# Performance work log

Hardware: AMD Instinct MI355X
Metric: run time of the kernel (lower is better)

Reference implementation:

```python
import jax, jax.numpy as jnp
import numpy as np

B, C, H, W = 64, 3, 64, 64
F = 96          # base_filters
K = 8           # n_mixtures
h, w = H // 2, W // 2
C0 = 2 * C      # channels of each checkerboard half
SECTIONS = [C0, C0, C0 * K, C0 * K, C0 * K]
SPLITS = [int(s) for s in np.cumsum(SECTIONS)[:-1]]
EPS = 1e-6


def conv2d(x, wgt, b):
    y = jax.lax.conv_general_dilated(x, wgt, (1, 1), 'SAME',
                                     dimension_numbers=('NCHW', 'OIHW', 'NCHW'))
    return y + b[None, :, None, None]


def layer_norm(x, g, b, eps=1e-5):
    # nn.LayerNorm(mid_shape): normalize over (C,H,W) per sample
    mu = jnp.mean(x, axis=(1, 2, 3), keepdims=True)
    var = jnp.var(x, axis=(1, 2, 3), keepdims=True)
    return (x - mu) / jnp.sqrt(var + eps) * g[None] + b[None]


def checker_split(z, odd=False):
    Bz, Cz, Hz, Wz = z.shape
    z = z.reshape(Bz, Cz, Hz // 2, 2, Wz // 2, 2)
    p00 = z[:, :, :, 0, :, 0]; p01 = z[:, :, :, 0, :, 1]
    p10 = z[:, :, :, 1, :, 0]; p11 = z[:, :, :, 1, :, 1]
    z0 = jnp.concatenate([p00, p11], axis=1)  # even checkerboard
    z1 = jnp.concatenate([p01, p10], axis=1)  # odd checkerboard
    if odd:
        z0, z1 = z1, z0
    return z0, z1


def checker_merge(z0, z1, odd=False):
    if odd:
        z0, z1 = z1, z0
    Cz = z0.shape[1] // 2
    p00, p11 = z0[:, :Cz], z0[:, Cz:]
    p01, p10 = z1[:, :Cz], z1[:, Cz:]
    Bz, _, hz, wz = p00.shape
    zi = jnp.stack([jnp.stack([p00, p01], axis=-1),
                    jnp.stack([p10, p11], axis=-1)], axis=-2)  # (B,C,h,w,2i,2j)
    z = zi.transpose(0, 1, 2, 4, 3, 5).reshape(Bz, Cz, 2 * hz, 2 * wz)
    return z


def gated_attn(x, qkv_w, qkv_b, proj_w, proj_b):
    Bx, Fx, hx, wx = x.shape
    xf = x.reshape(Bx, Fx, hx * wx).transpose(0, 2, 1)  # (B, L, F)
    qkv = xf @ qkv_w.T + qkv_b
    q, k, v = jnp.split(qkv, 3, axis=-1)
    scores = jnp.einsum('bqf,bkf->bqk', q, k) / jnp.sqrt(jnp.float32(Fx))
    attn = jax.nn.softmax(scores, axis=-1)
    o = jnp.einsum('bqk,bkf->bqf', attn, v)
    g = o @ proj_w.T + proj_b
    ga, gb = jnp.split(g, 2, axis=-1)
    out = xf + ga * jax.nn.sigmoid(gb)  # gated residual
    return out.transpose(0, 2, 1).reshape(Bx, Fx, hx, wx)


def conditioner(z1, conv1_w, conv1_b, gconv_w, gconv_b, ln1_g, ln1_b,
                qkv_w, qkv_b, proj_w, proj_b, ln2_g, ln2_b, conv2_w, conv2_b):
    x = conv2d(z1, conv1_w, conv1_b)
    g = conv2d(x, gconv_w, gconv_b)
    ga, gb = jnp.split(g, 2, axis=1)
    x = x + ga * jax.nn.sigmoid(gb)          # GatedConv2d
    x = layer_norm(x, ln1_g, ln1_b)
    x = gated_attn(x, qkv_w, qkv_b, proj_w, proj_b)
    x = layer_norm(x, ln2_g, ln2_b)
    return conv2d(x, conv2_w, conv2_b)


def _forward(z, log_df_dz, conv1_w, conv1_b, gconv_w, gconv_b, ln1_g, ln1_b,
             qkv_w, qkv_b, proj_w, proj_b, ln2_g, ln2_b, conv2_w, conv2_b,
             a_log_scale, a_bias):
    z0, z1 = checker_split(z)
    params = conditioner(z1, conv1_w, conv1_b, gconv_w, gconv_b, ln1_g, ln1_b,
                         qkv_w, qkv_b, proj_w, proj_b, ln2_g, ln2_b, conv2_w, conv2_b)
    a, b, logpi, mu, s = jnp.split(params, SPLITS, axis=1)
    a = jnp.tanh(a) * a_log_scale + a_bias
    Bz = z0.shape[0]
    logpi = jax.nn.log_softmax(logpi.reshape(Bz, K, C0, h, w), axis=1)
    mu = mu.reshape(Bz, K, C0, h, w)
    s = s.reshape(Bz, K, C0, h, w)
    # mixture-of-logistics CDF
    u = (z0[:, None] - mu) * jnp.exp(-s)
    x = jnp.sum(jnp.exp(logpi) * jax.nn.sigmoid(u), axis=1)
    log_pdf = jax.scipy.special.logsumexp(
        logpi - s + jax.nn.log_sigmoid(u) + jax.nn.log_sigmoid(-u), axis=1)
    log_df_dz = log_df_dz + jnp.sum(log_pdf.reshape(Bz, -1), axis=1)
    # logit transform
    x = jnp.clip(x, EPS, 1.0 - EPS)
    z0n = jnp.log(x) - jnp.log1p(-x)
    log_df_dz = log_df_dz + jnp.sum((-jnp.log(x) - jnp.log1p(-x)).reshape(Bz, -1), axis=1)
    # affine rescale
    z0n = z0n * jnp.exp(a) + b
    log_df_dz = log_df_dz + jnp.sum(a.reshape(Bz, -1), axis=1)
    return checker_merge(z0n, z1), log_df_dz


def setup_inputs() -> dict:
    key = jax.random.key(0)
    ks = jax.random.split(key, 10)
    sc = 0.05
    return dict(
        z=jax.random.normal(ks[0], (B, C, H, W), jnp.float32),
        log_df_dz=jnp.zeros((B,), jnp.float32),
        conv1_w=sc * jax.random.normal(ks[1], (F, C0, 3, 3), jnp.float32),
        conv1_b=jnp.zeros((F,), jnp.float32),
        gconv_w=sc * jax.random.normal(ks[2], (2 * F, F, 3, 3), jnp.float32),
        gconv_b=jnp.zeros((2 * F,), jnp.float32),
        ln1_g=jnp.ones((F, h, w), jnp.float32),
        ln1_b=jnp.zeros((F, h, w), jnp.float32),
        qkv_w=sc * jax.random.normal(ks[3], (3 * F, F), jnp.float32),
        qkv_b=jnp.zeros((3 * F,), jnp.float32),
        proj_w=sc * jax.random.normal(ks[4], (2 * F, F), jnp.float32),
        proj_b=jnp.zeros((2 * F,), jnp.float32),
        ln2_g=jnp.ones((F, h, w), jnp.float32),
        ln2_b=jnp.zeros((F, h, w), jnp.float32),
        conv2_w=sc * jax.random.normal(ks[5], (sum(SECTIONS), F, 3, 3), jnp.float32),
        conv2_b=jnp.zeros((sum(SECTIONS),), jnp.float32),
        a_log_scale=0.01 * jax.random.normal(ks[6], (1,), jnp.float32),
        a_bias=0.01 * jax.random.normal(ks[7], (1,), jnp.float32),
    )


def reference(z, log_df_dz, conv1_w, conv1_b, gconv_w, gconv_b, ln1_g, ln1_b,
              qkv_w, qkv_b, proj_w, proj_b, ln2_g, ln2_b, conv2_w, conv2_b,
              a_log_scale, a_bias):
    return _forward(z, log_df_dz, conv1_w, conv1_b, gconv_w, gconv_b, ln1_g, ln1_b,
                    qkv_w, qkv_b, proj_w, proj_b, ln2_g, ln2_b, conv2_w, conv2_b,
                    a_log_scale, a_bias)
```

## Files before the change

### kernel.cpp

```cpp
#include <hip/hip_runtime.h>
#include <cstdint>
#include <cstddef>


typedef unsigned short u16;
typedef __attribute__((ext_vector_type(8))) short short8;
typedef __attribute__((ext_vector_type(4))) float f32x4;

__device__ __forceinline__ float sigm(float x){ return 1.0f/(1.0f+__expf(-x)); }

__device__ __forceinline__ u16 f2bf(float f){
    unsigned int u = __float_as_uint(f);
    u += 0x7fffu + ((u >> 16) & 1u);
    return (u16)(u >> 16);
}
__device__ __forceinline__ float bf2f(u16 v){
    unsigned int u = ((unsigned int)v) << 16;
    return __uint_as_float(u);
}

__global__ __launch_bounds__(256) void k_prep(
    const float* __restrict__ z, const float* __restrict__ c1w, const float* __restrict__ c1b,
    const float* __restrict__ gw, const float* __restrict__ c2w,
    const float* __restrict__ qkvw, const float* __restrict__ pw,
    const float* __restrict__ ln1g, const float* __restrict__ ln1b,
    const float* __restrict__ ln2g, const float* __restrict__ ln2b,
    const float* __restrict__ logdf,
    u16* __restrict__ x1b,
    u16* __restrict__ Wg, u16* __restrict__ W2,
    u16* __restrict__ Wqkv, u16* __restrict__ Wproj,
    float* __restrict__ gt1, float* __restrict__ bt1,
    float* __restrict__ gt2, float* __restrict__ bt2,
    float* __restrict__ outlog)
{
    int blk = blockIdx.x;
    int tid = threadIdx.x;
    __shared__ float tin[6][6][34];
    __shared__ __align__(16) u16 Wc[96][72];
    __shared__ __align__(16) u16 imc[128][72];

    if (blk < 512){
        int b  = blk >> 3;
        int pg = blk & 7;
        int r0 = pg*4;
        for (int e = tid; e < 96*72; e += 256){
            int oc = e/72, k = e%72;
            Wc[oc][k] = (k < 54) ? f2bf(c1w[oc*54 + k]) : (u16)0;
        }
        for (int idx = tid; idx < 6*6*34; idx += 256){
            int c = idx/204, rem = idx%204;
            int rr = rem/34, q = rem%34;
            int ii = r0 - 1 + rr, jj = q - 1;
            float v = 0.f;
            if ((unsigned)ii < 32u && (unsigned)jj < 32u){
                if (c < 3) v = z[((b*3+c)*64 + 2*ii)*64 + (2*jj+1)];
                else       v = z[((b*3+(c-3))*64 + (2*ii+1))*64 + 2*jj];
            }
            tin[c][rr][q] = v;
        }
        __syncthreads();
        for (int e = tid; e < 128*72; e += 256){
            int px = e/72, k = e%72;
            float v = 0.f;
            if (k < 54){
                int c = k/9, rr = (k%9)/3, dcc = k%3;
                v = tin[c][(px>>5)+rr][(px&31)+dcc];
            }
            imc[px][k] = f2bf(v);
        }
        __syncthreads();

        int w = tid >> 6, lane = tid & 63;
        int cc = lane & 15, gg = lane >> 4;
        f32x4 acc[2][6];
        #pragma unroll
        for (int u=0;u<2;++u)
            #pragma unroll
            for (int t=0;t<6;++t) acc[u][t] = (f32x4){0.f,0.f,0.f,0.f};

        #pragma unroll
        for (int ks=0; ks<2; ++ks){
            short8 a0 = *reinterpret_cast<const short8*>(&imc[w*32 + cc     ][ks*32 + 8*gg]);
            short8 a1 = *reinterpret_cast<const short8*>(&imc[w*32 + 16 + cc][ks*32 + 8*gg]);
            #pragma unroll
            for (int t=0; t<6; ++t){
                short8 bb = *reinterpret_cast<const short8*>(&Wc[t*16+cc][ks*32 + 8*gg]);
                acc[0][t] = __builtin_amdgcn_mfma_f32_16x16x32_bf16(a0, bb, acc[0][t], 0,0,0);
                acc[1][t] = __builtin_amdgcn_mfma_f32_16x16x32_bf16(a1, bb, acc[1][t], 0,0,0);
            }
        }

        #pragma unroll
        for (int u=0;u<2;++u){
            int p0 = pg*128 + w*32 + u*16 + gg*4;
            #pragma unroll
            for (int t=0;t<6;++t){
                int oc = t*16+cc;
                float bv = c1b[oc];
                #pragma unroll
                for (int r=0;r<4;++r)
                    x1b[((size_t)(b*1024) + p0 + r)*96 + oc] = f2bf(acc[u][t][r] + bv);
            }
        }
    } else if (blk < 1160){
        int idx = (blk-512)*256 + tid;
        int tap = idx / (192*96);
        int rem = idx - tap*192*96;
        int ocp = rem / 96, ic = rem % 96;
        int obk = ocp/96, r = ocp%96, isB = r/48, i = r%48;
        int oc = obk*48 + i + isB*96;
        Wg[idx] = f2bf(gw[(size_t)(oc*96+ic)*9 + tap]);
    } else if (blk < 1700){
        int idx = (blk-1160)*256 + tid;
        int tap = idx / (160*96);
        int rem = idx - tap*160*96;
        int oc = rem / 96, ic = rem % 96;
        W2[idx] = (oc < 156) ? f2bf(c2w[(size_t)(oc*96+ic)*9 + tap]) : (u16)0;
    } else if (blk < 1808){
        int idx = (blk-1700)*256 + tid;
        Wqkv[idx] = f2bf(qkvw[idx]);
    } else if (blk < 1880){
        int idx = (blk-1808)*256 + tid;
        int ocp = idx / 96, ic = idx % 96;
        int obk = ocp/96, r = ocp%96, isB = r/48, i = r%48;
        int oc = obk*48 + i + isB*96;
        Wproj[idx] = f2bf(pw[(size_t)oc*96 + ic]);
    } else if (blk < 2264){
        int idx = (blk-1880)*256 + tid;
        int c = idx >> 10, p = idx & 1023;
        gt1[p*96 + c] = ln1g[idx];
    } else if (blk < 2648){
        int idx = (blk-2264)*256 + tid;
        int c = idx >> 10, p = idx & 1023;
        bt1[p*96 + c] = ln1b[idx];
    } else if (blk < 3032){
        int idx = (blk-2648)*256 + tid;
        int c = idx >> 10, p = idx & 1023;
        gt2[p*96 + c] = ln2g[idx];
    } else if (blk < 3416){
        int idx = (blk-3032)*256 + tid;
        int c = idx >> 10, p = idx & 1023;
        bt2[p*96 + c] = ln2b[idx];
    } else {
        if (tid < 64) outlog[tid] = logdf[tid];
    }
}

__global__ __launch_bounds__(256,4) void k_gconv(const u16* __restrict__ Xpb,
    const u16* __restrict__ Wt, const float* __restrict__ bias,
    u16* __restrict__ outb, float* __restrict__ partials)
{
    int blk  = blockIdx.x;
    int obk  = blk & 1;
    int pblk = (blk >> 1) & 7;
    int b    = blk >> 4;
    int tid  = threadIdx.x;
    int w = tid >> 6, lane = tid & 63;
    int cc = lane & 15, gg = lane >> 4;

    __shared__ __align__(16) u16 Ws[96][104];
    __shared__ float red[8];

    f32x4 acc[2][6];
    #pragma unroll
    for (int u=0;u<2;++u)
        #pragma unroll
        for (int t=0;t<6;++t) acc[u][t] = (f32x4){0.f,0.f,0.f,0.f};

    int base = pblk*128 + w*32;
    int ia = base >> 5;
    const u16* xb = Xpb + (size_t)b*1024*96;
    const u16* wbase = Wt + (size_t)obk*96*96;

    short8 wreg[5];
    #pragma unroll
    for (int i=0;i<5;++i){
        int c = tid + 256*i;
        if (c < 1152){
            int oc=c/12, ico=(c%12)*8;
            wreg[i] = *reinterpret_cast<const short8*>(wbase + oc*96 + ico);
        }
    }

    for (int tap=0; tap<9; ++tap){
        int dr = tap/3 - 1, dc = tap%3 - 1;
        __syncthreads();
        #pragma unroll
        for (int i=0;i<5;++i){
            int c = tid + 256*i;
            if (c < 1152){
                int oc=c/12, ico=(c%12)*8;
                *reinterpret_cast<short8*>(&Ws[oc][ico]) = wreg[i];
            }
        }
        if (tap < 8){
            const u16* wn = wbase + (size_t)(tap+1)*192*96;
            #pragma unroll
            for (int i=0;i<5;++i){
                int c = tid + 256*i;
                if (c < 1152){
                    int oc=c/12, ico=(c%12)*8;
                    wreg[i] = *reinterpret_cast<const short8*>(wn + oc*96 + ico);
                }
            }
        }
        __syncthreads();

        int ii = ia + dr;
        int jj0 = cc + dc, jj1 = cc + 16 + dc;
        bool rv = ((unsigned)ii < 32u);
        bool v0 = rv && ((unsigned)jj0 < 32u);
        bool v1 = rv && ((unsigned)jj1 < 32u);
        const u16* ar0 = xb + (ptrdiff_t)(ii*32 + jj0)*96 + 8*gg;
        const u16* ar1 = xb + (ptrdiff_t)(ii*32 + jj1)*96 + 8*gg;

        #pragma unroll
        for (int ks=0; ks<3; ++ks){
            short8 a0 = {0,0,0,0,0,0,0,0};
            short8 a1 = {0,0,0,0,0,0,0,0};
            if (v0) a0 = *reinterpret_cast<const short8*>(ar0 + ks*32);
            if (v1) a1 = *reinterpret_cast<const short8*>(ar1 + ks*32);
            #pragma unroll
            for (int t=0; t<6; ++t){
                short8 bb = *reinterpret_cast<const short8*>(&Ws[t*16+cc][ks*32+8*gg]);
                acc[0][t] = __builtin_amdgcn_mfma_f32_16x16x32_bf16(a0, bb, acc[0][t], 0,0,0);
                acc[1][t] = __builtin_amdgcn_mfma_f32_16x16x32_bf16(a1, bb, acc[1][t], 0,0,0);
            }
        }
    }

    float s = 0.f, ssq = 0.f;
    #pragma unroll
    for (int u=0;u<2;++u){
        int p0 = base + u*16 + gg*4;
        #pragma unroll
        for (int t=0;t<3;++t){
            int ocA = obk*48 + t*16+cc;
            float ba = bias[ocA], bbv = bias[ocA+96];
            #pragma unroll
            for (int r=0;r<4;++r){
                float res = bf2f(Xpb[((size_t)b*1024 + p0+r)*96 + ocA]);
                float va = acc[u][t][r]   + ba;
                float vb = acc[u][t+3][r] + bbv;
                float v = res + va*sigm(vb);
                outb[((size_t)b*1024 + p0+r)*96 + ocA] = f2bf(v);
                s += v; ssq += v*v;
            }
        }
    }
    #pragma unroll
    for (int o=32;o>0;o>>=1){ s += __shfl_down(s,o,64); ssq += __shfl_down(ssq,o,64); }
    if (lane==0){ red[w]=s; red[4+w]=ssq; }
    __syncthreads();
    if (tid==0){
        int slot = b*16 + pblk*2 + obk;
        partials[slot*2+0] = red[0]+red[1]+red[2]+red[3];
        partials[slot*2+1] = red[4]+red[5]+red[6]+red[7];
    }
}

__global__ __launch_bounds__(256) void k_lne(const u16* __restrict__ xb,
    const float* __restrict__ gt, const float* __restrict__ bt,
    const float* __restrict__ partials, u16* __restrict__ out)
{
    int b = blockIdx.x / 48, rem = blockIdx.x % 48;
    float s=0.f, ss=0.f;
    #pragma unroll
    for (int i=0;i<16;++i){ s += partials[(b*16+i)*2]; ss += partials[(b*16+i)*2+1]; }
    float mu = s/98304.f;
    float r = rsqrtf(ss/98304.f - mu*mu + 1e-5f);

    int e8 = rem*256 + threadIdx.x;
    size_t base = (size_t)b*98304 + (size_t)e8*8;
    short8 x8 = *reinterpret_cast<const short8*>(xb + base);
    const float* gp = gt + e8*8;
    const float* bp = bt + e8*8;
    short8 o8;
    #pragma unroll
    for (int i=0;i<8;++i)
        o8[i] = (short)f2bf((bf2f((u16)x8[i]) - mu)*r*gp[i] + bp[i]);
    *reinterpret_cast<short8*>(out + base) = o8;
}

__global__ __launch_bounds__(256,4) void k_conv2m(const u16* __restrict__ Xpb,
    const u16* __restrict__ Wt, const float* __restrict__ bias,
    u16* __restrict__ out)
{
    int blk  = blockIdx.x;
    int obk  = blk & 1;
    int pblk = (blk >> 1) & 7;
    int b    = blk >> 4;
    int tid  = threadIdx.x;
    int w = tid >> 6, lane = tid & 63;
    int cc = lane & 15, gg = lane >> 4;

    __shared__ __align__(16) u16 Ws[80][104];

    f32x4 acc[2][5];
    #pragma unroll
    for (int u=0;u<2;++u)
        #pragma unroll
        for (int t=0;t<5;++t) acc[u][t] = (f32x4){0.f,0.f,0.f,0.f};

    int base = pblk*128 + w*32;
    int ia = base >> 5;
    const u16* xb = Xpb + (size_t)b*1024*96;
    const u16* wbase = Wt + (size_t)obk*80*96;

    short8 wreg[4];
    #pragma unroll
    for (int i=0;i<4;++i){
        int c = tid + 256*i;
        if (c < 960){
            int oc=c/12, ico=(c%12)*8;
            wreg[i] = *reinterpret_cast<const short8*>(wbase + oc*96 + ico);
        }
    }

    for (int tap=0; tap<9; ++tap){
        int dr = tap/3 - 1, dc = tap%3 - 1;
        __syncthreads();
        #pragma unroll
        for (int i=0;i<4;++i){
            int c = tid + 256*i;
            if (c < 960){
                int oc=c/12, ico=(c%12)*8;
                *reinterpret_cast<short8*>(&Ws[oc][ico]) = wreg[i];
            }
        }
        if (tap < 8){
            const u16* wn = wbase + (size_t)(tap+1)*160*96;
            #pragma unroll
            for (int i=0;i<4;++i){
                int c = tid + 256*i;
                if (c < 960){
                    int oc=c/12, ico=(c%12)*8;
                    wreg[i] = *reinterpret_cast<const short8*>(wn + oc*96 + ico);
                }
            }
        }
        __syncthreads();

        int ii = ia + dr;
        int jj0 = cc + dc, jj1 = cc + 16 + dc;
        bool rv = ((unsigned)ii < 32u);
        bool v0 = rv && ((unsigned)jj0 < 32u);
        bool v1 = rv && ((unsigned)jj1 < 32u);
        const u16* ar0 = xb + (ptrdiff_t)(ii*32 + jj0)*96 + 8*gg;
        const u16* ar1 = xb + (ptrdiff_t)(ii*32 + jj1)*96 + 8*gg;

        #pragma unroll
        for (int ks=0; ks<3; ++ks){
            short8 a0 = {0,0,0,0,0,0,0,0};
            short8 a1 = {0,0,0,0,0,0,0,0};
            if (v0) a0 = *reinterpret_cast<const short8*>(ar0 + ks*32);
            if (v1) a1 = *reinterpret_cast<const short8*>(ar1 + ks*32);
            #pragma unroll
            for (int t=0; t<5; ++t){
                short8 bb = *reinterpret_cast<const short8*>(&Ws[t*16+cc][ks*32+8*gg]);
                acc[0][t] = __builtin_amdgcn_mfma_f32_16x16x32_bf16(a0, bb, acc[0][t], 0,0,0);
                acc[1][t] = __builtin_amdgcn_mfma_f32_16x16x32_bf16(a1, bb, acc[1][t], 0,0,0);
            }
        }
    }

    #pragma unroll
    for (int u=0;u<2;++u){
        int p0 = base + u*16 + gg*4;
        #pragma unroll
        for (int t=0;t<5;++t){
            int oc = obk*80 + t*16+cc;
            if (oc < 156){
                float bv = bias[oc];
                u16* op = out + ((size_t)b*156 + oc)*1024 + p0;
                #pragma unroll
                for (int r=0;r<4;++r) op[r] = f2bf(acc[u][t][r] + bv);
            }
        }
    }
}

__global__ __launch_bounds__(256,4) void k_qkvm(const u16* __restrict__ Xpb,
    const u16* __restrict__ Wt, const float* __restrict__ bias,
    u16* __restrict__ Qb, u16* __restrict__ Kf, u16* __restrict__ Vf)
{
    int blk  = blockIdx.x;
    int obk  = blk & 1;
    int pblk = (blk >> 1) & 7;
    int b    = blk >> 4;
    int tid  = threadIdx.x;
    int w = tid >> 6, lane = tid & 63;
    int cc = lane & 15, gg = lane >> 4;
    const float scale = 0.10206207262f;

    __shared__ __align__(16) u16 Ws[144][104];
    {
        const u16* wp = Wt + (size_t)obk*144*96;
        for (int c = tid; c < 144*12; c += 256){
            int oc = c/12, ico = (c%12)*8;
            *reinterpret_cast<short8*>(&Ws[oc][ico]) =
                *reinterpret_cast<const short8*>(wp + oc*96 + ico);
        }
    }

    f32x4 acc[2][9];
    #pragma unroll
    for (int u=0;u<2;++u)
        #pragma unroll
        for (int t=0;t<9;++t) acc[u][t] = (f32x4){0.f,0.f,0.f,0.f};

    int base = pblk*128 + w*32;
    const u16* xb = Xpb + ((size_t)b*1024 + base)*96;
    __syncthreads();

    #pragma unroll
    for (int ks=0; ks<3; ++ks){
        short8 a0 = *reinterpret_cast<const short8*>(xb + (size_t)cc*96      + ks*32 + 8*gg);
        short8 a1 = *reinterpret_cast<const short8*>(xb + (size_t)(cc+16)*96 + ks*32 + 8*gg);
        #pragma unroll
        for (int t=0; t<9; ++t){
            short8 bb = *reinterpret_cast<const short8*>(&Ws[t*16+cc][ks*32+8*gg]);
            acc[0][t] = __builtin_amdgcn_mfma_f32_16x16x32_bf16(a0, bb, acc[0][t], 0,0,0);
            acc[1][t] = __builtin_amdgcn_mfma_f32_16x16x32_bf16(a1, bb, acc[1][t], 0,0,0);
        }
    }

    #pragma unroll
    for (int u=0;u<2;++u){
        int p0 = base + u*16 + gg*4;
        #pragma unroll
        for (int t=0;t<9;++t){
            int n = obk*144 + t*16+cc;
            float bv = bias[n];
            #pragma unroll
            for (int r=0;r<4;++r){
                int p = p0 + r;
                float av = acc[u][t][r] + bv;
                if (n < 96){
                    Qb[((size_t)(b*1024+p))*96 + n] = f2bf(av*scale);
                } else if (n < 192){
                    int f = n-96;
                    int jt = p>>6, t16 = (p>>4)&3, ccs = p&15;
                    int ks = f>>5, ggs = (f>>3)&3, j = f&7;
                    Kf[(size_t)(b*16+jt)*6144 + (size_t)(((t16*3+ks)*4+ggs)*16+ccs)*8 + j] = f2bf(av);
                } else {
                    int f = n-192;
                    int jt = p>>6, kl = p&63;
                    int kk = kl>>5, ggs = (kl>>3)&3, j = kl&7;
                    int ft = f>>4, ccs = f&15;
                    Vf[(size_t)(b*16+jt)*6144 + (size_t)(((ft*2+kk)*4+ggs)*16+ccs)*8 + j] = f2bf(av);
                }
            }
        }
    }
}

__global__ __launch_bounds__(256,4) void k_attn(const u16* __restrict__ Qb,
    const u16* __restrict__ Kf, const u16* __restrict__ Vf, u16* __restrict__ Ob)
{
    int qt = blockIdx.x >> 6;
    int b  = blockIdx.x & 63;
    int tid = threadIdx.x;
    int w  = tid >> 6;
    int lane = tid & 63;
    int cc = lane & 15;
    int gg = lane >> 4;

    __shared__ __align__(16) u16 Ks[6144];
    __shared__ __align__(16) u16 Vs[6144];
    __shared__ __align__(16) u16 Ps[4][2048];

    int q0 = qt*64 + w*16;

    short8 qf[3];
    {
        const u16* qrow = Qb + ((size_t)(b*1024 + q0 + cc))*96;
        #pragma unroll
        for (int ks=0; ks<3; ++ks)
            qf[ks] = *reinterpret_cast<const short8*>(qrow + ks*32 + 8*gg);
    }

    f32x4 Oacc[6];
    #pragma unroll
    for (int ft=0; ft<6; ++ft) Oacc[ft] = (f32x4){0.f,0.f,0.f,0.f};
    float l_r[4] = {0.f,0.f,0.f,0.f};

    const u16* Kb0 = Kf + (size_t)(b*16)*6144;
    const u16* Vb0 = Vf + (size_t)(b*16)*6144;

    short8 kreg[3], vreg[3];
    #pragma unroll
    for (int i=0;i<3;++i){
        int s8 = (tid + 256*i)*8;
        kreg[i] = *reinterpret_cast<const short8*>(Kb0 + s8);
        vreg[i] = *reinterpret_cast<const short8*>(Vb0 + s8);
    }

    for (int jt=0; jt<16; ++jt){
        __syncthreads();
        #pragma unroll
        for (int i=0;i<3;++i){
            int s8 = (tid + 256*i)*8;
            *reinterpret_cast<short8*>(Ks + s8) = kreg[i];
            *reinterpret_cast<short8*>(Vs + s8) = vreg[i];
        }
        if (jt < 15){
            const u16* kn = Kb0 + (size_t)(jt+1)*6144;
            const u16* vn = Vb0 + (size_t)(jt+1)*6144;
            #pragma unroll
            for (int i=0;i<3;++i){
                int s8 = (tid + 256*i)*8;
                kreg[i] = *reinterpret_cast<const short8*>(kn + s8);
                vreg[i] = *reinterpret_cast<const short8*>(vn + s8);
            }
        }
        __syncthreads();

        f32x4 Sacc[4];
        #pragma unroll
        for (int t=0;t<4;++t) Sacc[t] = (f32x4){0.f,0.f,0.f,0.f};
        #pragma unroll
        for (int ks=0; ks<3; ++ks){
            #pragma unroll
            for (int t=0; t<4; ++t){
                short8 bb = *reinterpret_cast<const short8*>(Ks + ((t*3+ks)*64 + lane)*8);
                Sacc[t] = __builtin_amdgcn_mfma_f32_16x16x32_bf16(qf[ks], bb, Sacc[t], 0,0,0);
            }
        }

        #pragma unroll
        for (int t=0; t<4; ++t){
            int kk = t>>1;
            int ggs = ((t&1)<<1) | (cc>>3);
            int jj = cc&7;
            #pragma unroll
            for (int r=0; r<4; ++r){
                float p = __expf(Sacc[t][r]);
                l_r[r] += p;
                Ps[w][((kk*4 + ggs)*16 + (4*gg+r))*8 + jj] = f2bf(p);
            }
        }

        #pragma unroll
        for (int kk=0; kk<2; ++kk){
            short8 pa = *reinterpret_cast<const short8*>(&Ps[w][(kk*64 + lane)*8]);
            #pragma unroll
            for (int ft=0; ft<6; ++ft){
                short8 vb = *reinterpret_cast<const short8*>(Vs + ((ft*2+kk)*64 + lane)*8);
                Oacc[ft] = __builtin_amdgcn_mfma_f32_16x16x32_bf16(pa, vb, Oacc[ft], 0,0,0);
            }
        }
    }

    #pragma unroll
    for (int r=0; r<4; ++r){
        #pragma unroll
        for (int msk=1; msk<16; msk<<=1) l_r[r] += __shfl_xor(l_r[r], msk, 64);
    }
    float linv[4];
    #pragma unroll
    for (int r=0; r<4; ++r) linv[r] = 1.0f / l_r[r];
    #pragma unroll
    for (int ft=0; ft<6; ++ft)
        #pragma unroll
        for (int r=0; r<4; ++r)
            Ob[((size_t)(b*1024 + q0 + 4*gg + r))*96 + ft*16 + cc]
                = f2bf(Oacc[ft][r]*linv[r]);
}

__global__ __launch_bounds__(256,4) void k_projm(const u16* __restrict__ Opb,
    const u16* __restrict__ Wt, const float* __restrict__ bias,
    const u16* __restrict__ xlnb, u16* __restrict__ outb, float* __restrict__ partials)
{
    int blk  = blockIdx.x;
    int obk  = blk & 1;
    int pblk = (blk >> 1) & 7;
    int b    = blk >> 4;
    int tid  = threadIdx.x;
    int w = tid >> 6, lane = tid & 63;
    int cc = lane & 15, gg = lane >> 4;

    __shared__ __align__(16) u16 Ws[96][104];
    __shared__ float red[8];
    {
        const u16* wp = Wt + (size_t)obk*96*96;
        for (int c = tid; c < 96*12; c += 256){
            int oc = c/12, ico = (c%12)*8;
            *reinterpret_cast<short8*>(&Ws[oc][ico]) =
                *reinterpret_cast<const short8*>(wp + oc*96 + ico);
        }
    }

    f32x4 acc[2][6];
    #pragma unroll
    for (int u=0;u<2;++u)
        #pragma unroll
        for (int t=0;t<6;++t) acc[u][t] = (f32x4){0.f,0.f,0.f,0.f};

    int base = pblk*128 + w*32;
    const u16* xb = Opb + ((size_t)b*1024 + base)*96;
    __syncthreads();

    #pragma unroll
    for (int ks=0; ks<3; ++ks){
        short8 a0 = *reinterpret_cast<const short8*>(xb + (size_t)cc*96      + ks*32 + 8*gg);
        short8 a1 = *reinterpret_cast<const short8*>(xb + (size_t)(cc+16)*96 + ks*32 + 8*gg);
        #pragma unroll
        for (int t=0; t<6; ++t){
            short8 bb = *reinterpret_cast<const short8*>(&Ws[t*16+cc][ks*32+8*gg]);
            acc[0][t] = __builtin_amdgcn_mfma_f32_16x16x32_bf16(a0, bb, acc[0][t], 0,0,0);
            acc[1][t] = __builtin_amdgcn_mfma_f32_16x16x32_bf16(a1, bb, acc[1][t], 0,0,0);
        }
    }

    const u16* resb = xlnb + (size_t)b*1024*96;
    float s = 0.f, ssq = 0.f;
    #pragma unroll
    for (int u=0;u<2;++u){
        int p0 = base + u*16 + gg*4;
        #pragma unroll
        for (int t=0;t<3;++t){
            int ocA = obk*48 + t*16+cc;
            float ba = bias[ocA], bbv = bias[ocA+96];
            #pragma unroll
            for (int r=0;r<4;++r){
                float ga = acc[u][t][r]   + ba;
                float gb = acc[u][t+3][r] + bbv;
                float res = bf2f(resb[(size_t)(p0+r)*96 + ocA]);
                float v = res + ga * sigm(gb);
                outb[((size_t)b*1024 + p0+r)*96 + ocA] = f2bf(v);
                s += v; ssq += v*v;
            }
        }
    }
    #pragma unroll
    for (int o=32;o>0;o>>=1){ s += __shfl_down(s,o,64); ssq += __shfl_down(ssq,o,64); }
    if (lane==0){ red[w]=s; red[4+w]=ssq; }
    __syncthreads();
    if (tid==0){
        int slot = b*16 + pblk*2 + obk;
        partials[slot*2+0] = red[0]+red[1]+red[2]+red[3];
        partials[slot*2+1] = red[4]+red[5]+red[6]+red[7];
    }
}

__global__ __launch_bounds__(256) void k_mix(const float* __restrict__ z,
    const u16* __restrict__ params, const float* __restrict__ a_ls_p,
    const float* __restrict__ a_b_p, float* __restrict__ out_z, float* __restrict__ out_log)
{
    int b = blockIdx.x / 24;
    int rem = blockIdx.x % 24;
    int c0 = rem / 4;
    int pix = (rem & 3)*256 + threadIdx.x;
    int i = pix >> 5, j = pix & 31;
    float als = a_ls_p[0], abv = a_b_p[0];
    const u16* pb = params + (size_t)b*156*1024;
    float logacc = 0.f;

    if (c0 < 3){
        int idx01 = ((b*3+c0)*64 + 2*i)*64 + 2*j+1;
        int idx10 = ((b*3+c0)*64 + 2*i+1)*64 + 2*j;
        out_z[idx01] = z[idx01];
        out_z[idx10] = z[idx10];
    }

    {
        float z0v = (c0<3) ? z[((b*3+c0)*64 + 2*i)*64 + 2*j]
                           : z[((b*3+(c0-3))*64 + 2*i+1)*64 + 2*j+1];
        float a_raw = bf2f(pb[(c0)*1024 + pix]);
        float bco   = bf2f(pb[(6+c0)*1024 + pix]);
        float lp[8], mu[8], sv[8];
        float m1 = -1e30f;
        #pragma unroll
        for (int k=0;k<8;++k){
            lp[k] = bf2f(pb[(12 + k*6 + c0)*1024 + pix]);
            mu[k] = bf2f(pb[(60 + k*6 + c0)*1024 + pix]);
            sv[k] = bf2f(pb[(108 + k*6 + c0)*1024 + pix]);
            m1 = fmaxf(m1, lp[k]);
        }
        float se = 0.f;
        #pragma unroll
        for (int k=0;k<8;++k) se += __expf(lp[k]-m1);
        float lse = m1 + __logf(se);
        float xm = 0.f, mt = -1e30f;
        float t[8];
        #pragma unroll
        for (int k=0;k<8;++k){
            float lpn = lp[k] - lse;
            float u = (z0v - mu[k]) * __expf(-sv[k]);
            float au = fabsf(u);
            xm += __expf(lpn) * (1.f/(1.f+__expf(-u)));
            float lss = -(au + 2.f*log1pf(__expf(-au)));
            float tk = lpn - sv[k] + lss;
            t[k] = tk; mt = fmaxf(mt, tk);
        }
        float se2 = 0.f;
        #pragma unroll
        for (int k=0;k<8;++k) se2 += __expf(t[k]-mt);
        logacc += mt + __logf(se2);
        xm = fminf(fmaxf(xm, 1e-6f), 1.f-1e-6f);
        float lx = __logf(xm), l1x = log1pf(-xm);
        logacc += -lx - l1x;
        float aa = tanhf(a_raw)*als + abv;
        float z0n = (lx - l1x)*__expf(aa) + bco;
        logacc += aa;
        int oidx = (c0<3) ? ((b*3+c0)*64 + 2*i)*64 + 2*j
                          : ((b*3+(c0-3))*64 + 2*i+1)*64 + 2*j+1;
        out_z[oidx] = z0n;
    }

    #pragma unroll
    for (int o=32;o>0;o>>=1) logacc += __shfl_down(logacc, o, 64);
    __shared__ float part[4];
    if ((threadIdx.x&63)==0) part[threadIdx.x>>6] = logacc;
    __syncthreads();
    if (threadIdx.x==0){
        atomicAdd(out_log + b, part[0]+part[1]+part[2]+part[3]);
    }
}

extern "C" void kernel_launch(void* const* d_in, const int* in_sizes, int n_in,
                              void* d_out, int out_size, void* d_ws, size_t ws_size,
                              hipStream_t stream)
{
    const float* z     = (const float*)d_in[0];
    const float* logdf = (const float*)d_in[1];
    const float* c1w   = (const float*)d_in[2];
    const float* c1b   = (const float*)d_in[3];
    const float* gw    = (const float*)d_in[4];
    const float* gcb   = (const float*)d_in[5];
    const float* ln1g  = (const float*)d_in[6];
    const float* ln1b  = (const float*)d_in[7];
    const float* qkvw  = (const float*)d_in[8];
    const float* qkvb  = (const float*)d_in[9];
    const float* pw    = (const float*)d_in[10];
    const float* pbb   = (const float*)d_in[11];
    const float* ln2g  = (const float*)d_in[12];
    const float* ln2b  = (const float*)d_in[13];
    const float* c2w   = (const float*)d_in[14];
    const float* c2b   = (const float*)d_in[15];
    const float* als   = (const float*)d_in[16];
    const float* ab    = (const float*)d_in[17];

    float* out_z   = (float*)d_out;
    float* out_log = out_z + 786432;

    float* ws     = (float*)d_ws;
    u16*   x1b    = (u16*)(ws + 0);
    u16*   xg_b   = (u16*)(ws + 3145728);
    u16*   xlnb   = (u16*)(ws + 6291456);
    u16*   Vf     = (u16*)(ws + 9437184);
    u16*   Ob     = (u16*)(ws + 12582912);
    u16*   x2b    = (u16*)(ws + 15728640);
    u16*   Qb     = x1b;
    u16*   Kf     = xg_b;
    u16*   xln2b  = xlnb;
    u16*   params = (u16*)(ws + 9437184);
    const size_t T = 19660800;
    float* gt1    = ws + T;
    float* bt1    = ws + T + 98304;
    float* gt2    = ws + T + 196608;
    float* bt2    = ws + T + 294912;
    float* part1  = ws + T + 393216;
    float* part2  = ws + T + 395264;
    u16*   Wg     = (u16*)(ws + T + 397568);
    u16*   W2     = (u16*)(ws + T + 480512);
    u16*   Wqkv   = (u16*)(ws + T + 549632);
    u16*   Wproj  = (u16*)(ws + T + 563456);

    k_prep   <<<3417, 256, 0, stream>>>(z, c1w, c1b, gw, c2w, qkvw, pw,
                                        ln1g, ln1b, ln2g, ln2b, logdf,
                                        x1b, Wg, W2, Wqkv, Wproj,
                                        gt1, bt1, gt2, bt2, out_log);
    k_gconv  <<<1024, 256, 0, stream>>>(x1b, Wg, gcb, xg_b, part1);
    k_lne    <<<3072, 256, 0, stream>>>(xg_b, gt1, bt1, part1, xlnb);
    k_qkvm   <<<1024, 256, 0, stream>>>(xlnb, Wqkv, qkvb, Qb, Kf, Vf);
    k_attn   <<<1024, 256, 0, stream>>>(Qb, Kf, Vf, Ob);
    k_projm  <<<1024, 256, 0, stream>>>(Ob, Wproj, pbb, xlnb, x2b, part2);
    k_lne    <<<3072, 256, 0, stream>>>(x2b, gt2, bt2, part2, xln2b);
    k_conv2m <<<1024, 256, 0, stream>>>(xln2b, W2, c2b, params);
    k_mix    <<<1536, 256, 0, stream>>>(z, params, als, ab, out_z, out_log);
}
```

Before: 280.5 us.

## Restructure attention: 32 queries per wave, double-buffered K/V, register softmax packing

The attention kernel now handles 128 queries per block (32 per wave, two MFMA tiles sharing each K/V fragment load), which halves the grid. K/V tiles are double-buffered in LDS so one barrier per iteration is removed. The transposed-score MFMA layout plus permlane swaps pack softmax probabilities straight into registers instead of a round trip through LDS. Exp uses v_exp_f32 with log2e folded into the Q scale. Register pressure and occupancy drop (launch bounds 256,2), and the bf16 packing now rounds through a hardware convert.

Result: faster. 270.5 us (-3.6%).

```diff
diff --git a/kernel.cpp b/kernel.cpp
--- a/kernel.cpp
+++ b/kernel.cpp
@@ -6,6 +6,7 @@
 typedef unsigned short u16;
 typedef __attribute__((ext_vector_type(8))) short short8;
 typedef __attribute__((ext_vector_type(4))) float f32x4;
+typedef __attribute__((ext_vector_type(4))) unsigned int u32x4;
 
 __device__ __forceinline__ float sigm(float x){ return 1.0f/(1.0f+__expf(-x)); }
 
@@ -18,6 +19,42 @@
     unsigned int u = ((unsigned int)v) << 16;
     return __uint_as_float(u);
 }
+
+__device__ __forceinline__ float ex2(float x){
+    float r; asm("v_exp_f32 %0, %1" : "=v"(r) : "v"(x)); return r;
+}
+__device__ __forceinline__ unsigned cvtpk(float lo, float hi){
+    unsigned r; asm("v_cvt_pk_bf16_f32 %0, %1, %2" : "=v"(r) : "v"(lo), "v"(hi)); return r;
+}
+__device__ __forceinline__ void plswap32(unsigned &a, unsigned &b){
+    asm("v_permlane32_swap_b32 %0, %1" : "+v"(a), "+v"(b));
+}
+__device__ __forceinline__ void plswap16(unsigned &a, unsigned &b){
+    asm("v_permlane16_swap_b32 %0, %1" : "+v"(a), "+v"(b));
+}
+
+#define SOFTPACK(S, LACC, PA) do { \
+    unsigned pk_[4][2]; \
+    _Pragma("unroll") \
+    for (int t=0;t<4;++t){ \
+        float e0 = ex2(S[t][0]); \
+        float e1 = ex2(S[t][1]); \
+        float e2 = ex2(S[t][2]); \
+        float e3 = ex2(S[t][3]); \
+        LACC += (e0+e1)+(e2+e3); \
+        pk_[t][0] = cvtpk(e0,e1); \
+        pk_[t][1] = cvtpk(e2,e3); \
+    } \
+    _Pragma("unroll") \
+    for (int kk=0;kk<2;++kk){ \
+        unsigned a0 = pk_[2*kk][0], b0 = pk_[2*kk+1][0]; \
+        unsigned a1 = pk_[2*kk][1], b1 = pk_[2*kk+1][1]; \
+        plswap32(a0,b0); plswap16(a0,b0); \
+        plswap32(a1,b1); plswap16(a1,b1); \
+        u32x4 dw_; dw_[0]=a0; dw_[1]=a1; dw_[2]=b0; dw_[3]=b1; \
+        PA[kk] = __builtin_bit_cast(short8, dw_); \
+    } \
+} while(0)
 
 __global__ __launch_bounds__(256) void k_prep(
     const float* __restrict__ z, const float* __restrict__ c1w, const float* __restrict__ c1b,
@@ -391,7 +428,7 @@
     int tid  = threadIdx.x;
     int w = tid >> 6, lane = tid & 63;
     int cc = lane & 15, gg = lane >> 4;
-    const float scale = 0.10206207262f;
+    const float scale = 0.14724445f;
 
     __shared__ __align__(16) u16 Ws[144][104];
     {
@@ -455,7 +492,7 @@
     }
 }
 
-__global__ __launch_bounds__(256,4) void k_attn(const u16* __restrict__ Qb,
+__global__ __launch_bounds__(256,2) void k_attn(const u16* __restrict__ Qb,
     const u16* __restrict__ Kf, const u16* __restrict__ Vf, u16* __restrict__ Ob)
 {
     int qt = blockIdx.x >> 6;
@@ -466,24 +503,27 @@
     int cc = lane & 15;
     int gg = lane >> 4;
 
-    __shared__ __align__(16) u16 Ks[6144];
-    __shared__ __align__(16) u16 Vs[6144];
-    __shared__ __align__(16) u16 Ps[4][2048];
-
-    int q0 = qt*64 + w*16;
-
-    short8 qf[3];
+    __shared__ __align__(16) u16 Ks[2][6144];
+    __shared__ __align__(16) u16 Vs[2][6144];
+
+    int q0 = qt*128 + w*32;
+
+    short8 qf[2][3];
     {
-        const u16* qrow = Qb + ((size_t)(b*1024 + q0 + cc))*96;
-        #pragma unroll
-        for (int ks=0; ks<3; ++ks)
-            qf[ks] = *reinterpret_cast<const short8*>(qrow + ks*32 + 8*gg);
-    }
-
-    f32x4 Oacc[6];
-    #pragma unroll
-    for (int ft=0; ft<6; ++ft) Oacc[ft] = (f32x4){0.f,0.f,0.f,0.f};
-    float l_r[4] = {0.f,0.f,0.f,0.f};
+        const u16* qr0 = Qb + ((size_t)(b*1024 + q0 + cc))*96;
+        #pragma unroll
+        for (int ks=0; ks<3; ++ks){
+            qf[0][ks] = *reinterpret_cast<const short8*>(qr0 + ks*32 + 8*gg);
+            qf[1][ks] = *reinterpret_cast<const short8*>(qr0 + (size_t)16*96 + ks*32 + 8*gg);
+        }
+    }
+
+    f32x4 Oacc[2][6];
+    #pragma unroll
+    for (int u=0;u<2;++u)
+        #pragma unroll
+        for (int ft=0; ft<6; ++ft) Oacc[u][ft] = (f32x4){0.f,0.f,0.f,0.f};
+    float l_acc[2] = {0.f, 0.f};
 
     const u16* Kb0 = Kf + (size_t)(b*16)*6144;
     const u16* Vb0 = Vf + (size_t)(b*16)*6144;
@@ -495,18 +535,33 @@
         kreg[i] = *reinterpret_cast<const short8*>(Kb0 + s8);
         vreg[i] = *reinterpret_cast<const short8*>(Vb0 + s8);
     }
+    #pragma unroll
+    for (int i=0;i<3;++i){
+        int s8 = (tid + 256*i)*8;
+        *reinterpret_cast<short8*>(Ks[0] + s8) = kreg[i];
+        *reinterpret_cast<short8*>(Vs[0] + s8) = vreg[i];
+    }
+    #pragma unroll
+    for (int i=0;i<3;++i){
+        int s8 = (tid + 256*i)*8;
+        kreg[i] = *reinterpret_cast<const short8*>(Kb0 + 6144 + s8);
+        vreg[i] = *reinterpret_cast<const short8*>(Vb0 + 6144 + s8);
+    }
 
     for (int jt=0; jt<16; ++jt){
         __syncthreads();
-        #pragma unroll
-        for (int i=0;i<3;++i){
-            int s8 = (tid + 256*i)*8;
-            *reinterpret_cast<short8*>(Ks + s8) = kreg[i];
-            *reinterpret_cast<short8*>(Vs + s8) = vreg[i];
-        }
         if (jt < 15){
-            const u16* kn = Kb0 + (size_t)(jt+1)*6144;
-            const u16* vn = Vb0 + (size_t)(jt+1)*6144;
+            int nb = (jt+1)&1;
+            #pragma unroll
+            for (int i=0;i<3;++i){
+                int s8 = (tid + 256*i)*8;
+                *reinterpret_cast<short8*>(Ks[nb] + s8) = kreg[i];
+                *reinterpret_cast<short8*>(Vs[nb] + s8) = vreg[i];
+            }
+        }
+        if (jt < 14){
+            const u16* kn = Kb0 + (size_t)(jt+2)*6144;
+            const u16* vn = Vb0 + (size_t)(jt+2)*6144;
             #pragma unroll
             for (int i=0;i<3;++i){
                 int s8 = (tid + 256*i)*8;
@@ -514,58 +569,58 @@
                 vreg[i] = *reinterpret_cast<const short8*>(vn + s8);
             }
         }
-        __syncthreads();
-
-        f32x4 Sacc[4];
-        #pragma unroll
-        for (int t=0;t<4;++t) Sacc[t] = (f32x4){0.f,0.f,0.f,0.f};
+
+        const u16* Kc = Ks[jt&1];
+        const u16* Vc = Vs[jt&1];
+
+        f32x4 S0[4], S1[4];
+        #pragma unroll
+        for (int t=0;t<4;++t){ S0[t] = (f32x4){0.f,0.f,0.f,0.f}; S1[t] = (f32x4){0.f,0.f,0.f,0.f}; }
+
+        __builtin_amdgcn_s_setprio(1);
         #pragma unroll
         for (int ks=0; ks<3; ++ks){
             #pragma unroll
             for (int t=0; t<4; ++t){
-                short8 bb = *reinterpret_cast<const short8*>(Ks + ((t*3+ks)*64 + lane)*8);
-                Sacc[t] = __builtin_amdgcn_mfma_f32_16x16x32_bf16(qf[ks], bb, Sacc[t], 0,0,0);
-            }
-        }
-
-        #pragma unroll
-        for (int t=0; t<4; ++t){
-            int kk = t>>1;
-            int ggs = ((t&1)<<1) | (cc>>3);
-            int jj = cc&7;
-            #pragma unroll
-            for (int r=0; r<4; ++r){
-                float p = __expf(Sacc[t][r]);
-                l_r[r] += p;
-                Ps[w][((kk*4 + ggs)*16 + (4*gg+r))*8 + jj] = f2bf(p);
-            }
-        }
-
+                short8 kb = *reinterpret_cast<const short8*>(Kc + ((t*3+ks)*64 + lane)*8);
+                S0[t] = __builtin_amdgcn_mfma_f32_16x16x32_bf16(kb, qf[0][ks], S0[t], 0,0,0);
+                S1[t] = __builtin_amdgcn_mfma_f32_16x16x32_bf16(kb, qf[1][ks], S1[t], 0,0,0);
+            }
+        }
+        __builtin_amdgcn_s_setprio(0);
+
+        short8 pa0[2], pa1[2];
+        SOFTPACK(S0, l_acc[0], pa0);
+        SOFTPACK(S1, l_acc[1], pa1);
+
+        __builtin_amdgcn_s_setprio(1);
         #pragma unroll
         for (int kk=0; kk<2; ++kk){
-            short8 pa = *reinterpret_cast<const short8*>(&Ps[w][(kk*64 + lane)*8]);
             #pragma unroll
             for (int ft=0; ft<6; ++ft){
-                short8 vb = *reinterpret_cast<const short8*>(Vs + ((ft*2+kk)*64 + lane)*8);
-                Oacc[ft] = __builtin_amdgcn_mfma_f32_16x16x32_bf16(pa, vb, Oacc[ft], 0,0,0);
-            }
-        }
-    }
-
-    #pragma unroll
-    for (int r=0; r<4; ++r){
-        #pragma unroll
-        for (int msk=1; msk<16; msk<<=1) l_r[r] += __shfl_xor(l_r[r], msk, 64);
-    }
-    float linv[4];
-    #pragma unroll
-    for (int r=0; r<4; ++r) linv[r] = 1.0f / l_r[r];
-    #pragma unroll
-    for (int ft=0; ft<6; ++ft)
-        #pragma unroll
-        for (int r=0; r<4; ++r)
-            Ob[((size_t)(b*1024 + q0 + 4*gg + r))*96 + ft*16 + cc]
-                = f2bf(Oacc[ft][r]*linv[r]);
+                short8 vb = *reinterpret_cast<const short8*>(Vc + ((ft*2+kk)*64 + lane)*8);
+                Oacc[0][ft] = __builtin_amdgcn_mfma_f32_16x16x32_bf16(pa0[kk], vb, Oacc[0][ft], 0,0,0);
+                Oacc[1][ft] = __builtin_amdgcn_mfma_f32_16x16x32_bf16(pa1[kk], vb, Oacc[1][ft], 0,0,0);
+            }
+        }
+        __builtin_amdgcn_s_setprio(0);
+    }
+
+    #pragma unroll
+    for (int u=0;u<2;++u){
+        float lv = l_acc[u];
+        lv += __shfl_xor(lv, 16, 64);
+        lv += __shfl_xor(lv, 32, 64);
+        float linv[4];
+        #pragma unroll
+        for (int r=0;r<4;++r) linv[r] = 1.0f / __shfl(lv, 4*gg + r, 64);
+        #pragma unroll
+        for (int ft=0; ft<6; ++ft)
+            #pragma unroll
+            for (int r=0; r<4; ++r)
+                Ob[((size_t)(b*1024 + q0 + u*16 + 4*gg + r))*96 + ft*16 + cc]
+                    = f2bf(Oacc[u][ft][r]*linv[r]);
+    }
 }
 
 __global__ __launch_bounds__(256,4) void k_projm(const u16* __restrict__ Opb,
@@ -775,7 +830,7 @@
     k_gconv  <<<1024, 256, 0, stream>>>(x1b, Wg, gcb, xg_b, part1);
     k_lne    <<<3072, 256, 0, stream>>>(xg_b, gt1, bt1, part1, xlnb);
     k_qkvm   <<<1024, 256, 0, stream>>>(xlnb, Wqkv, qkvb, Qb, Kf, Vf);
-    k_attn   <<<1024, 256, 0, stream>>>(Qb, Kf, Vf, Ob);
+    k_attn   <<<512, 256, 0, stream>>>(Qb, Kf, Vf, Ob);
     k_projm  <<<1024, 256, 0, stream>>>(Ob, Wproj, pbb, xlnb, x2b, part2);
     k_lne    <<<3072, 256, 0, stream>>>(x2b, gt2, bt2, part2, xln2b);
     k_conv2m <<<1024, 256, 0, stream>>>(xln2b, W2, c2b, params);
```
